# Performance work log

Hardware: AMD Instinct MI355X
Metric: run time of the kernel (lower is better)

## Reference

```python
import jax, jax.numpy as jnp
import numpy as np

B, T, I, U, M = 256, 8192, 6, 64, 16
ODE_UNFOLDS = 6
ELAPSED = 1.0
EPS = 1e-8


def setup_inputs() -> dict:
    key = jax.random.key(0)
    ks = jax.random.split(key, 12)
    x = jax.random.normal(ks[0], (B, T, I), dtype=jnp.float32)
    # LTCCell parameters (ncps-style init ranges)
    gleak = jax.random.uniform(ks[1], (U,), minval=0.001, maxval=1.0)
    vleak = jax.random.uniform(ks[2], (U,), minval=-0.2, maxval=0.2)
    cm = jax.random.uniform(ks[3], (U,), minval=0.4, maxval=0.6)
    sigma = jax.random.uniform(ks[4], (U, U), minval=3.0, maxval=8.0)
    mu = jax.random.uniform(ks[5], (U, U), minval=0.3, maxval=0.8)
    w = jax.random.uniform(ks[6], (U, U), minval=0.001, maxval=1.0)
    erev = jnp.where(jax.random.uniform(ks[7], (U, U)) < 0.5, -1.0, 1.0)
    sensory_sigma = jax.random.uniform(ks[8], (I, U), minval=3.0, maxval=8.0)
    sensory_mu = jax.random.uniform(ks[9], (I, U), minval=0.3, maxval=0.8)
    sensory_w = jax.random.uniform(ks[10], (I, U), minval=0.001, maxval=1.0)
    sensory_erev = jnp.where(jax.random.uniform(ks[11], (I, U)) < 0.5, -1.0, 1.0)
    input_w = jnp.ones((I,), jnp.float32)
    input_b = jnp.zeros((I,), jnp.float32)
    output_w = jnp.ones((M,), jnp.float32)
    output_b = jnp.zeros((M,), jnp.float32)
    return {
        "x": x, "gleak": gleak, "vleak": vleak, "cm": cm,
        "sigma": sigma, "mu": mu, "w": w, "erev": erev,
        "sensory_sigma": sensory_sigma, "sensory_mu": sensory_mu,
        "sensory_w": sensory_w, "sensory_erev": sensory_erev,
        "input_w": input_w, "input_b": input_b,
        "output_w": output_w, "output_b": output_b,
    }


def reference(x, gleak, vleak, cm, sigma, mu, w, erev,
              sensory_sigma, sensory_mu, sensory_w, sensory_erev,
              input_w, input_b, output_w, output_b):
    # DgaRawSequence: unroll LTCCell over time with zero-initialized hidden state.
    cm_t = cm / (ELAPSED / ODE_UNFOLDS)  # [U]
    xs = jnp.swapaxes(x, 0, 1)  # [T, B, I]

    def step(v, xt):
        # map_inputs (affine per-feature)
        xi = xt * input_w + input_b  # [B, I]
        # sensory synapse activations, constant across ODE unfolds
        sw = sensory_w * jax.nn.sigmoid((xi[:, :, None] - sensory_mu) * sensory_sigma)  # [B,I,U]
        num_s = jnp.sum(sw * sensory_erev, axis=1)  # [B, U]
        den_s = jnp.sum(sw, axis=1)                 # [B, U]
        # fused semi-implicit Euler ODE solver
        for _ in range(ODE_UNFOLDS):
            wa = w * jax.nn.sigmoid((v[:, :, None] - mu) * sigma)  # [B,U,U]
            num = cm_t * v + gleak * vleak + jnp.sum(wa * erev, axis=1) + num_s
            den = cm_t + gleak + jnp.sum(wa, axis=1) + den_s
            v = num / (den + EPS)
        # map_outputs: first M (motor) neurons, affine
        out = v[:, :M] * output_w + output_b  # [B, M]
        return v, out

    v0 = jnp.zeros((x.shape[0], U), x.dtype)
    _, outs = jax.lax.scan(step, v0, xs)  # outs: [T, B, M]
    return jnp.swapaxes(outs, 0, 1)  # [B, T, M]
```

## Files before the change

kernel.cpp:

```cpp
#include <hip/hip_runtime.h>

#define NB 256
#define NT 8192
#define NI 6
#define NU 64
#define NM 16
#define UNFOLDS 6
#define EPSF 1e-8f
#define LOG2E 1.44269504088896340736f

typedef float v2f __attribute__((ext_vector_type(2)));

__device__ __forceinline__ float fexp2(float x) { return __builtin_amdgcn_exp2f(x); }
__device__ __forceinline__ float frcp(float x)  { return __builtin_amdgcn_rcpf(x); }

template <int CTRL>
__device__ __forceinline__ float dpp_add(float x) {
  int t = __builtin_amdgcn_update_dpp(0, __float_as_int(x), CTRL, 0xF, 0xF, true);
  return x + __int_as_float(t);
}
__device__ __forceinline__ float red8(float x) {
  x = dpp_add<0xB1>(x);
  x = dpp_add<0x4E>(x);
  x = dpp_add<0x141>(x);
  return x;
}

__device__ __forceinline__ void lds_barrier() {
  asm volatile("s_waitcnt lgkmcnt(0)\n\ts_barrier" ::: "memory");
}

__global__ __launch_bounds__(512, 2) void ltc_kernel(
    const float* __restrict__ x,
    const float* __restrict__ gleak, const float* __restrict__ vleak,
    const float* __restrict__ cm,
    const float* __restrict__ sigma, const float* __restrict__ mu,
    const float* __restrict__ w,     const float* __restrict__ erev,
    const float* __restrict__ ssigma, const float* __restrict__ smu,
    const float* __restrict__ sw_,    const float* __restrict__ serev,
    const float* __restrict__ iw, const float* __restrict__ ib,
    const float* __restrict__ ow_, const float* __restrict__ ob_,
    float* __restrict__ out)
{
  const int tid = threadIdx.x;
  const int b   = blockIdx.x;
  const int j   = tid >> 3;
  const int c   = tid & 7;
  const int i0  = c * 8;

  v2f a1p[4], a0p[4], wq[8];
#pragma unroll
  for (int k = 0; k < 8; ++k) {
    const int idx = (i0 + k) * NU + j;
    const float sg = sigma[idx] * LOG2E;
    a1p[k >> 1][k & 1] = -sg;
    a0p[k >> 1][k & 1] = mu[idx] * sg;
    const float wvk = w[idx];
    wq[k] = (v2f){wvk * erev[idx], wvk};
  }
  float b1 = 0.f, b0 = 0.f, swv = 0.f, swe = 0.f;
  if (c < NI) {
    const int idx = c * NU + j;
    const float sg = ssigma[idx] * LOG2E;
    b1 = -sg * iw[c];
    b0 = sg * (smu[idx] - ib[c]);
    swv = sw_[idx];
    swe = swv * serev[idx];
  }
  const float gl   = gleak[j];
  const float glvl = gl * vleak[j];
  const float cmt  = cm[j] * (float)UNFOLDS;
  const float ow   = (j < NM) ? ow_[j] : 0.f;
  const float ob   = (j < NM) ? ob_[j] : 0.f;

  __shared__ float vbuf[2][NU];
  float v = 0.f;
  if (c == 0) vbuf[0][j] = 0.f;
  __syncthreads();

  const float* xp = x + (size_t)b * NT * NI + (c < NI ? c : 0);
  float* op = out + (size_t)b * NT * NM;

  auto sens_seed = [&](float xv) -> v2f {
    const float es   = fexp2(fmaf(xv, b1, b0));
    const float ssig = frcp(1.f + es);
    const float num_s = red8(swe * ssig);
    const float den_s = red8(swv * ssig);
    return (v2f){(glvl + num_s) * 0.125f,
                 (cmt + gl + den_s + EPSF) * 0.125f};
  };

  v2f seedA = sens_seed(xp[0]);
  float xv_nxt = xp[NI];
  v2f seedB;

  auto unfold_step = [&](int p) {
    float vv[8];
    *(float4*)&vv[0] = *(const float4*)&vbuf[p][i0];
    *(float4*)&vv[4] = *(const float4*)&vbuf[p][i0 + 4];
    v2f vp2[4] = { {vv[0], vv[1]}, {vv[2], vv[3]}, {vv[4], vv[5]}, {vv[6], vv[7]} };

    v2f accA = seedA, accB = (v2f){0.f, 0.f};
#pragma unroll
    for (int q = 0; q < 4; ++q) {
      const v2f y = vp2[q] * a1p[q] + a0p[q];
      const float e0 = fexp2(y.x);
      const float e1 = fexp2(y.y);
      const float d0 = 1.f + e0;
      const float d1 = 1.f + e1;
      const float r  = frcp(d0 * d1);
      v2f tq = wq[2 * q] * d1 + wq[2 * q + 1] * d0;
      if (q & 1) accB += tq * r; else accA += tq * r;
    }
    const v2f acc = accA + accB;
    const float an = red8(acc.x);
    const float ad = red8(acc.y);
    v = fmaf(cmt, v, an) * frcp(ad);
    if (c == 0) vbuf[p ^ 1][j] = v;
    lds_barrier();
  };

  for (int t = 0; t < NT; ++t) {
    const int tn = (t + 2 < NT) ? (t + 2) : (NT - 1);
    const float xf = xp[tn * NI];

    unfold_step(0);
    seedB = sens_seed(xv_nxt);
    unfold_step(1);
    unfold_step(0);
    unfold_step(1);
    unfold_step(0);
    unfold_step(1);

    if (c == 0 && j < NM) op[t * NM + j] = fmaf(v, ow, ob);

    seedA = seedB;
    xv_nxt = xf;
  }
}

extern "C" void kernel_launch(void* const* d_in, const int* in_sizes, int n_in,
                              void* d_out, int out_size, void* d_ws, size_t ws_size,
                              hipStream_t stream) {
  (void)in_sizes; (void)n_in; (void)d_ws; (void)ws_size; (void)out_size;
  const float* x      = (const float*)d_in[0];
  const float* gleak  = (const float*)d_in[1];
  const float* vleak  = (const float*)d_in[2];
  const float* cm     = (const float*)d_in[3];
  const float* sigma  = (const float*)d_in[4];
  const float* mu     = (const float*)d_in[5];
  const float* w      = (const float*)d_in[6];
  const float* erev   = (const float*)d_in[7];
  const float* ssig   = (const float*)d_in[8];
  const float* smu    = (const float*)d_in[9];
  const float* sw     = (const float*)d_in[10];
  const float* serev  = (const float*)d_in[11];
  const float* iw     = (const float*)d_in[12];
  const float* ib     = (const float*)d_in[13];
  const float* ow     = (const float*)d_in[14];
  const float* ob     = (const float*)d_in[15];
  float* out = (float*)d_out;

  ltc_kernel<<<dim3(NB), dim3(512), 0, stream>>>(
      x, gleak, vleak, cm, sigma, mu, w, erev,
      ssig, smu, sw, serev, iw, ib, ow, ob, out);
}
```

Baseline: 15.77 ms.

## Use 4 lanes per neuron with 256-thread blocks instead of 8 lanes

Regroups the per-neuron work so each thread handles 16 presynaptic inputs with 4 lanes per neuron instead of 8 inputs across 8 lanes. The block shrinks to 256 threads, the cross-lane reduction drops from three DPP steps to two, and the per-step barrier synchronises fewer wavefronts. Sensory inputs are split two per lane. The trade-off is doubled serial exp/rcp work per thread on the latency-critical recurrence.

```diff
diff --git a/kernel.cpp b/kernel.cpp
--- a/kernel.cpp
+++ b/kernel.cpp
@@ -19,10 +19,9 @@
   int t = __builtin_amdgcn_update_dpp(0, __float_as_int(x), CTRL, 0xF, 0xF, true);
   return x + __int_as_float(t);
 }
-__device__ __forceinline__ float red8(float x) {
+__device__ __forceinline__ float red4(float x) {
   x = dpp_add<0xB1>(x);
   x = dpp_add<0x4E>(x);
-  x = dpp_add<0x141>(x);
   return x;
 }
 
@@ -30,7 +29,7 @@
   asm volatile("s_waitcnt lgkmcnt(0)\n\ts_barrier" ::: "memory");
 }
 
-__global__ __launch_bounds__(512, 2) void ltc_kernel(
+__global__ __launch_bounds__(256, 1) void ltc_kernel(
     const float* __restrict__ x,
     const float* __restrict__ gleak, const float* __restrict__ vleak,
     const float* __restrict__ cm,
@@ -44,13 +43,13 @@
 {
   const int tid = threadIdx.x;
   const int b   = blockIdx.x;
-  const int j   = tid >> 3;
-  const int c   = tid & 7;
-  const int i0  = c * 8;
+  const int j   = tid >> 2;
+  const int c   = tid & 3;
+  const int i0  = c * 16;
 
-  v2f a1p[4], a0p[4], wq[8];
+  v2f a1p[8], a0p[8], wq[16];
 #pragma unroll
-  for (int k = 0; k < 8; ++k) {
+  for (int k = 0; k < 16; ++k) {
     const int idx = (i0 + k) * NU + j;
     const float sg = sigma[idx] * LOG2E;
     a1p[k >> 1][k & 1] = -sg;
@@ -58,14 +57,25 @@
     const float wvk = w[idx];
     wq[k] = (v2f){wvk * erev[idx], wvk};
   }
-  float b1 = 0.f, b0 = 0.f, swv = 0.f, swe = 0.f;
-  if (c < NI) {
-    const int idx = c * NU + j;
-    const float sg = ssigma[idx] * LOG2E;
-    b1 = -sg * iw[c];
-    b0 = sg * (smu[idx] - ib[c]);
-    swv = sw_[idx];
-    swe = swv * serev[idx];
+  float b1a = 0.f, b0a = 0.f, swva = 0.f, swea = 0.f;
+  float b1b = 0.f, b0b = 0.f, swvb = 0.f, sweb = 0.f;
+  {
+    const int ia = c;
+    const int idxa = ia * NU + j;
+    const float sga = ssigma[idxa] * LOG2E;
+    b1a = -sga * iw[ia];
+    b0a = sga * (smu[idxa] - ib[ia]);
+    swva = sw_[idxa];
+    swea = swva * serev[idxa];
+    if (c < 2) {
+      const int ib2 = c + 4;
+      const int idxb = ib2 * NU + j;
+      const float sgb = ssigma[idxb] * LOG2E;
+      b1b = -sgb * iw[ib2];
+      b0b = sgb * (smu[idxb] - ib[ib2]);
+      swvb = sw_[idxb];
+      sweb = swvb * serev[idxb];
+    }
   }
   const float gl   = gleak[j];
   const float glvl = gl * vleak[j];
@@ -78,32 +88,40 @@
   if (c == 0) vbuf[0][j] = 0.f;
   __syncthreads();
 
-  const float* xp = x + (size_t)b * NT * NI + (c < NI ? c : 0);
+  const float* xpA = x + (size_t)b * NT * NI + c;
+  const float* xpB = x + (size_t)b * NT * NI + ((c < 2) ? (c + 4) : 0);
   float* op = out + (size_t)b * NT * NM;
 
-  auto sens_seed = [&](float xv) -> v2f {
-    const float es   = fexp2(fmaf(xv, b1, b0));
-    const float ssig = frcp(1.f + es);
-    const float num_s = red8(swe * ssig);
-    const float den_s = red8(swv * ssig);
-    return (v2f){(glvl + num_s) * 0.125f,
-                 (cmt + gl + den_s + EPSF) * 0.125f};
+  auto sens_seed = [&](float xa, float xb) -> v2f {
+    const float e0 = fexp2(fmaf(xa, b1a, b0a));
+    const float e1 = fexp2(fmaf(xb, b1b, b0b));
+    const float d0 = 1.f + e0;
+    const float d1 = 1.f + e1;
+    const float r  = frcp(d0 * d1);
+    const float s0 = d1 * r;
+    const float s1 = d0 * r;
+    const float num_s = red4(fmaf(swea, s0, sweb * s1));
+    const float den_s = red4(fmaf(swva, s0, swvb * s1));
+    return (v2f){(glvl + num_s) * 0.25f,
+                 (cmt + gl + den_s + EPSF) * 0.25f};
   };
 
-  v2f seedA = sens_seed(xp[0]);
-  float xv_nxt = xp[NI];
+  v2f seedA = sens_seed(xpA[0], xpB[0]);
+  float xvA_nxt = xpA[NI];
+  float xvB_nxt = xpB[NI];
   v2f seedB;
 
   auto unfold_step = [&](int p) {
-    float vv[8];
-    *(float4*)&vv[0] = *(const float4*)&vbuf[p][i0];
-    *(float4*)&vv[4] = *(const float4*)&vbuf[p][i0 + 4];
-    v2f vp2[4] = { {vv[0], vv[1]}, {vv[2], vv[3]}, {vv[4], vv[5]}, {vv[6], vv[7]} };
+    float vv[16];
+    *(float4*)&vv[0]  = *(const float4*)&vbuf[p][i0];
+    *(float4*)&vv[4]  = *(const float4*)&vbuf[p][i0 + 4];
+    *(float4*)&vv[8]  = *(const float4*)&vbuf[p][i0 + 8];
+    *(float4*)&vv[12] = *(const float4*)&vbuf[p][i0 + 12];
 
     v2f accA = seedA, accB = (v2f){0.f, 0.f};
 #pragma unroll
-    for (int q = 0; q < 4; ++q) {
-      const v2f y = vp2[q] * a1p[q] + a0p[q];
+    for (int q = 0; q < 8; ++q) {
+      const v2f y = (v2f){vv[2 * q], vv[2 * q + 1]} * a1p[q] + a0p[q];
       const float e0 = fexp2(y.x);
       const float e1 = fexp2(y.y);
       const float d0 = 1.f + e0;
@@ -113,8 +131,8 @@
       if (q & 1) accB += tq * r; else accA += tq * r;
     }
     const v2f acc = accA + accB;
-    const float an = red8(acc.x);
-    const float ad = red8(acc.y);
+    const float an = red4(acc.x);
+    const float ad = red4(acc.y);
     v = fmaf(cmt, v, an) * frcp(ad);
     if (c == 0) vbuf[p ^ 1][j] = v;
     lds_barrier();
@@ -122,10 +140,11 @@
 
   for (int t = 0; t < NT; ++t) {
     const int tn = (t + 2 < NT) ? (t + 2) : (NT - 1);
-    const float xf = xp[tn * NI];
+    const float xfA = xpA[tn * NI];
+    const float xfB = xpB[tn * NI];
 
     unfold_step(0);
-    seedB = sens_seed(xv_nxt);
+    seedB = sens_seed(xvA_nxt, xvB_nxt);
     unfold_step(1);
     unfold_step(0);
     unfold_step(1);
@@ -135,7 +154,8 @@
     if (c == 0 && j < NM) op[t * NM + j] = fmaf(v, ow, ob);
 
     seedA = seedB;
-    xv_nxt = xf;
+    xvA_nxt = xfA;
+    xvB_nxt = xfB;
   }
 }
 
@@ -161,7 +181,7 @@
   const float* ob     = (const float*)d_in[15];
   float* out = (float*)d_out;
 
-  ltc_kernel<<<dim3(NB), dim3(512), 0, stream>>>(
+  ltc_kernel<<<dim3(NB), dim3(256), 0, stream>>>(
       x, gleak, vleak, cm, sigma, mu, w, erev,
       ssig, smu, sw, serev, iw, ib, ow, ob, out);
 }
```

Result: no change. 15.69 ms (-0.5%).
